# Kernel tuning notes

Measured on AMD Instinct MI355X. Metric: run time of the kernel, lower is better.

## Reference

```python
import jax, jax.numpy as jnp
import numpy as np

B, D, K = 8, 128, 7          # batch, num objects, per-object feature
Q = 256                      # question embedding size
G0, G1 = 511, 512            # g-layer sizes
F1, F2, OUT = 512, 1024, 16  # f-layer sizes


def setup_inputs() -> dict:
    key = jax.random.key(0)
    ks = jax.random.split(key, 14)
    def lin(kw, kb, fan_in, fan_out):
        lim = 1.0 / np.sqrt(fan_in)
        w = jax.random.uniform(kw, (fan_in, fan_out), jnp.float32, -lim, lim)
        b = jax.random.uniform(kb, (fan_out,), jnp.float32, -lim, lim)
        return w, b
    x = jax.random.normal(ks[0], (B, D, K), jnp.float32)
    qst = jax.random.normal(ks[1], (B, Q), jnp.float32)
    g0_w, g0_b = lin(ks[2], ks[3], 2 * K, G0)
    g1_w, g1_b = lin(ks[4], ks[5], G0 + Q, G1)
    f1_w, f1_b = lin(ks[6], ks[7], G1, F1)
    f2_w, f2_b = lin(ks[8], ks[9], F1, F2)
    f3_w, f3_b = lin(ks[10], ks[11], F2, OUT)
    return {"x": x, "qst": qst,
            "g0_w": g0_w, "g0_b": g0_b, "g1_w": g1_w, "g1_b": g1_b,
            "f1_w": f1_w, "f1_b": f1_b, "f2_w": f2_w, "f2_b": f2_b,
            "f3_w": f3_w, "f3_b": f3_b}


def reference(x, qst, g0_w, g0_b, g1_w, g1_b, f1_w, f1_b, f2_w, f2_b, f3_w, f3_b):
    b, d, k = x.shape
    # all-pairs: torch x_i[b,a,c,:]=x[b,c,:], x_j[b,a,c,:]=x[b,a,:]
    x_i = jnp.broadcast_to(x[:, None, :, :], (b, d, d, k))
    x_j = jnp.broadcast_to(x[:, :, None, :], (b, d, d, k))
    pairs = jnp.concatenate([x_i, x_j], axis=-1)            # (b,d,d,2k)
    h = jax.nn.relu(pairs @ g0_w + g0_b)                    # (b,d,d,G0)
    q = jnp.broadcast_to(qst[:, None, None, :], (b, d, d, qst.shape[-1]))
    h = jnp.concatenate([h, q], axis=-1)                    # (b,d,d,G0+Q)
    h = jax.nn.relu(h @ g1_w + g1_b)                        # (b,d,d,G1)
    x_g = h.sum(axis=(1, 2))                                # sum over d^2 pairs -> (b,G1)
    f = jax.nn.relu(x_g @ f1_w + f1_b)
    f = jax.nn.relu(f @ f2_w + f2_b)                        # dropout = identity (eval)
    logits = f @ f3_w + f3_b
    return jax.nn.log_softmax(logits, axis=1)
```

## Files before the change

kernel.cpp:

```cpp
#include <hip/hip_runtime.h>
#include <hip/hip_bf16.h>

#define B_  8
#define D_  128
#define K_  7
#define Q_  256
#define G0_ 511
#define G0P 512
#define G1_ 512
#define F1_ 512
#define F2_ 1024
#define OUT_ 16

typedef __bf16 bf16x8 __attribute__((ext_vector_type(8)));
typedef float  f32x4  __attribute__((ext_vector_type(4)));

#define GL2LDS(g, l) __builtin_amdgcn_global_load_lds(                        \
    (const __attribute__((address_space(1))) void*)(g),                       \
    (__attribute__((address_space(3))) void*)(l), 16, 0, 0)

__global__ void k_prep(const float* __restrict__ x, const float* __restrict__ g0w,
                       const float* __restrict__ g0b, const float* __restrict__ qst,
                       const float* __restrict__ g1w, const float* __restrict__ g1b,
                       const float* __restrict__ f1w, const float* __restrict__ f2w,
                       const float* __restrict__ f3w,
                       float* __restrict__ u, float* __restrict__ v,
                       __bf16* __restrict__ w1t, float* __restrict__ qterm,
                       float* __restrict__ xg, float* __restrict__ f1t,
                       float* __restrict__ f2t, float* __restrict__ f3t) {
    const int blk = blockIdx.x;
    const int t   = threadIdx.x;
    if (blk < 1024) {
        __shared__ float xs[8];
        if (t < K_) xs[t] = x[blk * K_ + t];
        __syncthreads();
        #pragma unroll
        for (int h = 0; h < 2; ++h) {
            const int g = t + h * 256;
            float su = 0.f, sv = 0.f;
            if (g < G0_) {
                #pragma unroll
                for (int k = 0; k < K_; ++k) {
                    su += xs[k] * g0w[k * G0_ + g];
                    sv += xs[k] * g0w[(K_ + k) * G0_ + g];
                }
                su += g0b[g];
            }
            u[blk * G0P + g] = (g < G0_) ? su : 0.f;
            v[blk * G0P + g] = (g < G0_) ? sv : 0.f;
        }
    } else if (blk < 1280) {
        __shared__ __bf16 tile[32][33];
        const int bb = blk - 1024;
        const int bx = bb & 15, by = bb >> 4;
        const int r = t >> 5, c = t & 31;
        #pragma unroll
        for (int i = 0; i < 4; ++i) {
            const int k = by * 32 + r + i * 8;
            const int n = bx * 32 + c;
            tile[r + i * 8][c] = (__bf16)((k < G0_) ? g1w[k * G1_ + n] : 0.f);
        }
        __syncthreads();
        #pragma unroll
        for (int i = 0; i < 4; ++i) {
            const int n = bx * 32 + r + i * 8;
            const int cc = (c >> 3) & 3, j = c & 7;
            const int slot = cc ^ ((n >> 1) & 3);
            w1t[by * 16384 + n * 32 + slot * 8 + j] = tile[c][r + i * 8];
        }
    } else if (blk < 1312) {
        __shared__ float qs[256];
        __shared__ float red[2][128];
        const int qb = blk - 1280;
        const int b = qb >> 2, nb = (qb & 3) << 7;
        qs[t] = qst[b * Q_ + t];
        __syncthreads();
        const int n = nb + (t & 127);
        const int qh = (t >> 7) * 128;
        float s = 0.f;
        #pragma unroll 8
        for (int q = 0; q < 128; ++q)
            s += qs[qh + q] * g1w[(G0_ + qh + q) * G1_ + n];
        red[t >> 7][t & 127] = s;
        __syncthreads();
        if (t < 128)
            qterm[b * G1_ + nb + t] = red[0][t] + red[1][t] + g1b[nb + t];
    } else if (blk < 1320) {
        const int b = blk - 1312;
        xg[b * G1_ + t] = 0.f;
        xg[b * G1_ + 256 + t] = 0.f;
    } else if (blk < 1576) {
        __shared__ float tile[32][33];
        const int j = blk - 1320;
        const int bo = j & 15, bk = j >> 4;
        const int r = t >> 5, c = t & 31;
        #pragma unroll
        for (int i = 0; i < 4; ++i)
            tile[r + i * 8][c] = f1w[(bk * 32 + r + i * 8) * F1_ + bo * 32 + c];
        __syncthreads();
        #pragma unroll
        for (int i = 0; i < 4; ++i)
            f1t[(bo * 32 + r + i * 8) * G1_ + bk * 32 + c] = tile[c][r + i * 8];
    } else if (blk < 2088) {
        __shared__ float tile[32][33];
        const int j = blk - 1576;
        const int bo = j & 31, bk = j >> 5;
        const int r = t >> 5, c = t & 31;
        #pragma unroll
        for (int i = 0; i < 4; ++i)
            tile[r + i * 8][c] = f2w[(bk * 32 + r + i * 8) * F2_ + bo * 32 + c];
        __syncthreads();
        #pragma unroll
        for (int i = 0; i < 4; ++i)
            f2t[(bo * 32 + r + i * 8) * F1_ + bk * 32 + c] = tile[c][r + i * 8];
    } else {
        const int k = (blk - 2088) * 256 + t;
        float4 r0 = *(const float4*)(f3w + k * OUT_);
        float4 r1 = *(const float4*)(f3w + k * OUT_ + 4);
        float4 r2 = *(const float4*)(f3w + k * OUT_ + 8);
        float4 r3 = *(const float4*)(f3w + k * OUT_ + 12);
        const float rr[16] = {r0.x,r0.y,r0.z,r0.w, r1.x,r1.y,r1.z,r1.w,
                              r2.x,r2.y,r2.z,r2.w, r3.x,r3.y,r3.z,r3.w};
        #pragma unroll
        for (int o = 0; o < 16; ++o) f3t[o * F2_ + k] = rr[o];
    }
}

__global__ __launch_bounds__(512, 4)
void k_pair(const float* __restrict__ u, const float* __restrict__ v,
            const __bf16* __restrict__ w1t, const float* __restrict__ qterm,
            float* __restrict__ xg) {
    __shared__ float  v_a[512];
    __shared__ __bf16 At[2][4096];
    __shared__ __bf16 Bt[3][8192];
    __shared__ float  ebuf[8][64];

    const int bid  = blockIdx.x;
    const int b    = bid >> 8;
    const int a    = (bid >> 1) & 127;
    const int nbase = (bid & 1) << 8;
    const int tid  = threadIdx.x;
    const int wave = tid >> 6, lane = tid & 63;
    const int quad = lane >> 4, l15 = lane & 15;
    const int wm   = wave >> 2;
    const int wn   = wave & 3;
    const int nloc = wn * 64;
    const int mtg  = wm * 4;
    const int swz  = (l15 >> 1) & 3;

    const int iw0 = wave * 2;
    const __bf16* gsrc = w1t + (size_t)(nbase + iw0 * 16 + (lane >> 2)) * 32
                             + (lane & 3) * 8;

    const int sm = tid >> 2;
    const int q8 = tid & 3;
    const float* urow = u + (size_t)(b * D_ + sm) * G0P + q8 * 8;
    const int woff = ((sm >> 4) * 512 + q8 * 128 + (sm & 15) * 8)
                   ^ (((q8 << 1) | ((sm >> 3) & 1)) << 3);
    const int afoff = (lane ^ (lane >> 3)) * 8;

    f32x4 acc[4][4];
    #pragma unroll
    for (int mt = 0; mt < 4; ++mt)
        #pragma unroll
        for (int nt = 0; nt < 4; ++nt)
            acc[mt][nt] = (f32x4){0.f, 0.f, 0.f, 0.f};

    float4 ua, ub;
    auto load_u = [&](int kq) {
        const float* p = urow + kq * 32;
        ua = *(const float4*)p;
        ub = *(const float4*)(p + 4);
    };
    auto stage_B = [&](int buf, int kq) {
        const __bf16* g = gsrc + (size_t)kq * 16384;
        __bf16* l = &Bt[buf][iw0 * 512];
        GL2LDS(g, l);
        GL2LDS(g + 512, l + 512);
    };
    auto write_A = [&](int buf, int kq) {
        const float* vp = v_a + kq * 32 + q8 * 8;
        const float4 va = *(const float4*)vp;
        const float4 vb = *(const float4*)(vp + 4);
        bf16x8 h;
        h[0] = (__bf16)fmaxf(ua.x + va.x, 0.f);
        h[1] = (__bf16)fmaxf(ua.y + va.y, 0.f);
        h[2] = (__bf16)fmaxf(ua.z + va.z, 0.f);
        h[3] = (__bf16)fmaxf(ua.w + va.w, 0.f);
        h[4] = (__bf16)fmaxf(ub.x + vb.x, 0.f);
        h[5] = (__bf16)fmaxf(ub.y + vb.y, 0.f);
        h[6] = (__bf16)fmaxf(ub.z + vb.z, 0.f);
        h[7] = (__bf16)fmaxf(ub.w + vb.w, 0.f);
        *(bf16x8*)&At[buf][woff] = h;
    };

    float4 vq;
    if (tid < 128) vq = *(const float4*)(v + (b * D_ + a) * G0P + tid * 4);
    load_u(0);
    asm volatile("" ::: "memory");
    stage_B(0, 0);
    stage_B(1, 1);
    if (tid < 128) *(float4*)(v_a + tid * 4) = vq;
    asm volatile("s_waitcnt lgkmcnt(0)\n\ts_barrier" ::: "memory");
    write_A(0, 0);
    asm volatile("s_waitcnt vmcnt(2) lgkmcnt(0)\n\ts_barrier" ::: "memory");

    int bcur = 0, bnxt = 1, bstg = 2;
    for (int kq = 0; kq < 16; ++kq) {
        const int abuf = kq & 1;
        if (kq < 15) load_u(kq + 1);
        asm volatile("" ::: "memory");
        if (kq < 14) stage_B(bstg, kq + 2);

        bf16x8 af[4];
        const __bf16* atb = &At[abuf][mtg * 512 + afoff];
        #pragma unroll
        for (int mt = 0; mt < 4; ++mt)
            af[mt] = *(const bf16x8*)(atb + mt * 512);
        bf16x8 bfr[4];
        const __bf16* btb = &Bt[bcur][(nloc + l15) * 32 + ((quad ^ swz) << 3)];
        #pragma unroll
        for (int nt = 0; nt < 4; ++nt)
            bfr[nt] = *(const bf16x8*)(btb + nt * 512);
        __builtin_amdgcn_s_setprio(1);
        #pragma unroll
        for (int mt = 0; mt < 4; ++mt)
            #pragma unroll
            for (int nt = 0; nt < 4; ++nt)
                acc[mt][nt] = __builtin_amdgcn_mfma_f32_16x16x32_bf16(
                    af[mt], bfr[nt], acc[mt][nt], 0, 0, 0);
        __builtin_amdgcn_s_setprio(0);

        if (kq < 15) write_A(abuf ^ 1, kq + 1);
        asm volatile("s_waitcnt lgkmcnt(0)\n\ts_barrier" ::: "memory");
        const int t3 = bcur; bcur = bnxt; bnxt = bstg; bstg = t3;
    }

    #pragma unroll
    for (int nt = 0; nt < 4; ++nt) {
        const float q = qterm[b * G1_ + nbase + nloc + nt * 16 + l15];
        float s = 0.f;
        #pragma unroll
        for (int mt = 0; mt < 4; ++mt)
            #pragma unroll
            for (int r = 0; r < 4; ++r)
                s += fmaxf(acc[mt][nt][r] + q, 0.f);
        s += __shfl_xor(s, 16, 64);
        s += __shfl_xor(s, 32, 64);
        if (quad == 0) ebuf[wave][nt * 16 + l15] = s;
    }
    __syncthreads();
    if (tid < 256) {
        const float sv = ebuf[tid >> 6][tid & 63] + ebuf[4 + (tid >> 6)][tid & 63];
        atomicAdd(xg + b * G1_ + nbase + tid, sv);
    }
}

__global__ void k_f1(const float* __restrict__ xg, const float* __restrict__ f1t,
                     const float* __restrict__ f1b, float* __restrict__ s1g) {
    const int wave = threadIdx.x >> 6, lane = threadIdx.x & 63;
    const int id = blockIdx.x * 4 + wave;
    const int b = id >> 9, oo = id & 511;
    const float* xr = xg + b * G1_ + lane * 8;
    const float* wr = f1t + oo * G1_ + lane * 8;
    const float4 a0 = *(const float4*)xr, a1 = *(const float4*)(xr + 4);
    const float4 b0 = *(const float4*)wr, b1 = *(const float4*)(wr + 4);
    float s = a0.x*b0.x + a0.y*b0.y + a0.z*b0.z + a0.w*b0.w
            + a1.x*b1.x + a1.y*b1.y + a1.z*b1.z + a1.w*b1.w;
    #pragma unroll
    for (int off = 32; off >= 1; off >>= 1) s += __shfl_xor(s, off, 64);
    if (lane == 0) s1g[b * F1_ + oo] = fmaxf(s + f1b[oo], 0.f);
}

__global__ void k_f2(const float* __restrict__ s1g, const float* __restrict__ f2t,
                     const float* __restrict__ f2b, float* __restrict__ s2g) {
    const int wave = threadIdx.x >> 6, lane = threadIdx.x & 63;
    const int id = blockIdx.x * 4 + wave;
    const int b = id >> 10, oo = id & 1023;
    const float* xr = s1g + b * F1_ + lane * 8;
    const float* wr = f2t + oo * F1_ + lane * 8;
    const float4 a0 = *(const float4*)xr, a1 = *(const float4*)(xr + 4);
    const float4 b0 = *(const float4*)wr, b1 = *(const float4*)(wr + 4);
    float s = a0.x*b0.x + a0.y*b0.y + a0.z*b0.z + a0.w*b0.w
            + a1.x*b1.x + a1.y*b1.y + a1.z*b1.z + a1.w*b1.w;
    #pragma unroll
    for (int off = 32; off >= 1; off >>= 1) s += __shfl_xor(s, off, 64);
    if (lane == 0) s2g[b * F2_ + oo] = fmaxf(s + f2b[oo], 0.f);
}

__global__ void k_f3(const float* __restrict__ s2g, const float* __restrict__ f3t,
                     const float* __restrict__ f3b, float* __restrict__ out) {
    const int b = blockIdx.x, t = threadIdx.x;
    const int wave = t >> 6, lane = t & 63;
    __shared__ float lg[16];
    float4 xs[4];
    #pragma unroll
    for (int j = 0; j < 4; ++j)
        xs[j] = *(const float4*)(s2g + b * F2_ + lane * 16 + j * 4);
    #pragma unroll
    for (int oi = 0; oi < 4; ++oi) {
        const int o = wave * 4 + oi;
        const float* wr = f3t + o * F2_ + lane * 16;
        float s = 0.f;
        #pragma unroll
        for (int j = 0; j < 4; ++j) {
            const float4 w = *(const float4*)(wr + j * 4);
            s += xs[j].x*w.x + xs[j].y*w.y + xs[j].z*w.z + xs[j].w*w.w;
        }
        #pragma unroll
        for (int off = 32; off >= 1; off >>= 1) s += __shfl_xor(s, off, 64);
        if (lane == 0) lg[o] = s + f3b[o];
    }
    __syncthreads();
    if (t < 16) {
        float m = -1e30f;
        #pragma unroll
        for (int i = 0; i < 16; ++i) m = fmaxf(m, lg[i]);
        float se = 0.f;
        #pragma unroll
        for (int i = 0; i < 16; ++i) se += __expf(lg[i] - m);
        out[b * OUT_ + t] = lg[t] - m - logf(se);
    }
}

extern "C" void kernel_launch(void* const* d_in, const int* in_sizes, int n_in,
                              void* d_out, int out_size, void* d_ws, size_t ws_size,
                              hipStream_t stream) {
    const float* x   = (const float*)d_in[0];
    const float* qst = (const float*)d_in[1];
    const float* g0w = (const float*)d_in[2];
    const float* g0b = (const float*)d_in[3];
    const float* g1w = (const float*)d_in[4];
    const float* g1b = (const float*)d_in[5];
    const float* f1w = (const float*)d_in[6];
    const float* f1b = (const float*)d_in[7];
    const float* f2w = (const float*)d_in[8];
    const float* f2b = (const float*)d_in[9];
    const float* f3w = (const float*)d_in[10];
    const float* f3b = (const float*)d_in[11];

    char* ws = (char*)d_ws;
    float*  u     = (float*)ws;  ws += (size_t)B_ * D_ * G0P * 4;
    float*  v     = (float*)ws;  ws += (size_t)B_ * D_ * G0P * 4;
    __bf16* w1t   = (__bf16*)ws; ws += (size_t)G1_ * G0P * 2;
    float*  qterm = (float*)ws;  ws += (size_t)B_ * G1_ * 4;
    float*  xg    = (float*)ws;  ws += (size_t)B_ * G1_ * 4;
    float*  s1g   = (float*)ws;  ws += (size_t)B_ * F1_ * 4;
    float*  s2g   = (float*)ws;  ws += (size_t)B_ * F2_ * 4;
    float*  f1t   = (float*)ws;  ws += (size_t)F1_ * G1_ * 4;
    float*  f2t   = (float*)ws;  ws += (size_t)F2_ * F1_ * 4;
    float*  f3t   = (float*)ws;  ws += (size_t)OUT_ * F2_ * 4;

    k_prep<<<2092, 256, 0, stream>>>(x, g0w, g0b, qst, g1w, g1b, f1w, f2w, f3w,
                                     u, v, w1t, qterm, xg, f1t, f2t, f3t);
    k_pair<<<B_ * D_ * 2, 512, 0, stream>>>(u, v, w1t, qterm, xg);
    k_f1  <<<1024, 256, 0, stream>>>(xg, f1t, f1b, s1g);
    k_f2  <<<2048, 256, 0, stream>>>(s1g, f2t, f2b, s2g);
    k_f3  <<<B_, 256, 0, stream>>>(s2g, f3t, f3b, (float*)d_out);
}
```

Measured before the change: 172.9 us.

## Fuse f1/f2/f3 tail kernels into one cooperative kernel with grid sync

Replaces the three small MLP-tail launches with a single cooperative kernel of 128 blocks of 1024 threads that runs f1, grid-syncs, runs f2, grid-syncs, then computes f3 and the log-softmax in 8 blocks. The aim is to remove the launch gaps and per-kernel drain between the tiny tail stages. In exchange it adds grid-wide barrier cost and fewer waves per stage, and it relies on cooperative launch support and all blocks being co-resident.

Measured after the change: 228.6 us. +32.2%, slower.

```diff
diff --git a/kernel.cpp b/kernel.cpp
--- a/kernel.cpp
+++ b/kernel.cpp
@@ -1,5 +1,7 @@
 #include <hip/hip_runtime.h>
 #include <hip/hip_bf16.h>
+#include <hip/hip_cooperative_groups.h>
+namespace cg = cooperative_groups;
 
 #define B_  8
 #define D_  128
@@ -256,70 +258,76 @@
     }
 }
 
-__global__ void k_f1(const float* __restrict__ xg, const float* __restrict__ f1t,
-                     const float* __restrict__ f1b, float* __restrict__ s1g) {
-    const int wave = threadIdx.x >> 6, lane = threadIdx.x & 63;
-    const int id = blockIdx.x * 4 + wave;
-    const int b = id >> 9, oo = id & 511;
-    const float* xr = xg + b * G1_ + lane * 8;
-    const float* wr = f1t + oo * G1_ + lane * 8;
-    const float4 a0 = *(const float4*)xr, a1 = *(const float4*)(xr + 4);
-    const float4 b0 = *(const float4*)wr, b1 = *(const float4*)(wr + 4);
-    float s = a0.x*b0.x + a0.y*b0.y + a0.z*b0.z + a0.w*b0.w
-            + a1.x*b1.x + a1.y*b1.y + a1.z*b1.z + a1.w*b1.w;
+__global__ __launch_bounds__(1024)
+void k_ftail(const float* __restrict__ xg,
+             const float* __restrict__ f1t, const float* __restrict__ f1b,
+             const float* __restrict__ f2t, const float* __restrict__ f2b,
+             const float* __restrict__ f3t, const float* __restrict__ f3b,
+             float* __restrict__ s1g, float* __restrict__ s2g,
+             float* __restrict__ out) {
+    cg::grid_group grid = cg::this_grid();
+    const int tid  = threadIdx.x;
+    const int wave = tid >> 6, lane = tid & 63;
+    const int gw   = blockIdx.x * 16 + wave;
+
     #pragma unroll
-    for (int off = 32; off >= 1; off >>= 1) s += __shfl_xor(s, off, 64);
-    if (lane == 0) s1g[b * F1_ + oo] = fmaxf(s + f1b[oo], 0.f);
-}
-
-__global__ void k_f2(const float* __restrict__ s1g, const float* __restrict__ f2t,
-                     const float* __restrict__ f2b, float* __restrict__ s2g) {
-    const int wave = threadIdx.x >> 6, lane = threadIdx.x & 63;
-    const int id = blockIdx.x * 4 + wave;
-    const int b = id >> 10, oo = id & 1023;
-    const float* xr = s1g + b * F1_ + lane * 8;
-    const float* wr = f2t + oo * F1_ + lane * 8;
-    const float4 a0 = *(const float4*)xr, a1 = *(const float4*)(xr + 4);
-    const float4 b0 = *(const float4*)wr, b1 = *(const float4*)(wr + 4);
-    float s = a0.x*b0.x + a0.y*b0.y + a0.z*b0.z + a0.w*b0.w
-            + a1.x*b1.x + a1.y*b1.y + a1.z*b1.z + a1.w*b1.w;
+    for (int r = 0; r < 2; ++r) {
+        const int id = gw + r * 2048;
+        const int b = id >> 9, oo = id & 511;
+        const float* xr = xg + b * G1_ + lane * 8;
+        const float* wr = f1t + (size_t)oo * G1_ + lane * 8;
+        const float4 a0 = *(const float4*)xr, a1 = *(const float4*)(xr + 4);
+        const float4 b0 = *(const float4*)wr, b1 = *(const float4*)(wr + 4);
+        float s = a0.x*b0.x + a0.y*b0.y + a0.z*b0.z + a0.w*b0.w
+                + a1.x*b1.x + a1.y*b1.y + a1.z*b1.z + a1.w*b1.w;
+        #pragma unroll
+        for (int off = 32; off >= 1; off >>= 1) s += __shfl_xor(s, off, 64);
+        if (lane == 0) s1g[b * F1_ + oo] = fmaxf(s + f1b[oo], 0.f);
+    }
+    grid.sync();
+
     #pragma unroll
-    for (int off = 32; off >= 1; off >>= 1) s += __shfl_xor(s, off, 64);
-    if (lane == 0) s2g[b * F2_ + oo] = fmaxf(s + f2b[oo], 0.f);
-}
-
-__global__ void k_f3(const float* __restrict__ s2g, const float* __restrict__ f3t,
-                     const float* __restrict__ f3b, float* __restrict__ out) {
-    const int b = blockIdx.x, t = threadIdx.x;
-    const int wave = t >> 6, lane = t & 63;
-    __shared__ float lg[16];
-    float4 xs[4];
-    #pragma unroll
-    for (int j = 0; j < 4; ++j)
-        xs[j] = *(const float4*)(s2g + b * F2_ + lane * 16 + j * 4);
-    #pragma unroll
-    for (int oi = 0; oi < 4; ++oi) {
-        const int o = wave * 4 + oi;
-        const float* wr = f3t + o * F2_ + lane * 16;
+    for (int r = 0; r < 4; ++r) {
+        const int id = gw + r * 2048;
+        const int b = id >> 10, oo = id & 1023;
+        const float* xr = s1g + b * F1_ + lane * 8;
+        const float* wr = f2t + (size_t)oo * F1_ + lane * 8;
+        const float4 a0 = *(const float4*)xr, a1 = *(const float4*)(xr + 4);
+        const float4 b0 = *(const float4*)wr, b1 = *(const float4*)(wr + 4);
+        float s = a0.x*b0.x + a0.y*b0.y + a0.z*b0.z + a0.w*b0.w
+                + a1.x*b1.x + a1.y*b1.y + a1.z*b1.z + a1.w*b1.w;
+        #pragma unroll
+        for (int off = 32; off >= 1; off >>= 1) s += __shfl_xor(s, off, 64);
+        if (lane == 0) s2g[b * F2_ + oo] = fmaxf(s + f2b[oo], 0.f);
+    }
+    grid.sync();
+
+    if (blockIdx.x < 8) {
+        const int b = blockIdx.x;
+        __shared__ float lg[16];
+        const int o = wave;
+        const float* xr = s2g + b * F2_ + lane * 16;
+        const float* wr = f3t + (size_t)o * F2_ + lane * 16;
         float s = 0.f;
         #pragma unroll
         for (int j = 0; j < 4; ++j) {
-            const float4 w = *(const float4*)(wr + j * 4);
-            s += xs[j].x*w.x + xs[j].y*w.y + xs[j].z*w.z + xs[j].w*w.w;
+            const float4 xv = *(const float4*)(xr + j * 4);
+            const float4 wv = *(const float4*)(wr + j * 4);
+            s += xv.x*wv.x + xv.y*wv.y + xv.z*wv.z + xv.w*wv.w;
         }
         #pragma unroll
         for (int off = 32; off >= 1; off >>= 1) s += __shfl_xor(s, off, 64);
         if (lane == 0) lg[o] = s + f3b[o];
-    }
-    __syncthreads();
-    if (t < 16) {
-        float m = -1e30f;
-        #pragma unroll
-        for (int i = 0; i < 16; ++i) m = fmaxf(m, lg[i]);
-        float se = 0.f;
-        #pragma unroll
-        for (int i = 0; i < 16; ++i) se += __expf(lg[i] - m);
-        out[b * OUT_ + t] = lg[t] - m - logf(se);
+        __syncthreads();
+        if (tid < 16) {
+            float m = -1e30f;
+            #pragma unroll
+            for (int i = 0; i < 16; ++i) m = fmaxf(m, lg[i]);
+            float se = 0.f;
+            #pragma unroll
+            for (int i = 0; i < 16; ++i) se += __expf(lg[i] - m);
+            out[b * OUT_ + tid] = lg[tid] - m - logf(se);
+        }
     }
 }
 
@@ -354,7 +362,11 @@
     k_prep<<<2092, 256, 0, stream>>>(x, g0w, g0b, qst, g1w, g1b, f1w, f2w, f3w,
                                      u, v, w1t, qterm, xg, f1t, f2t, f3t);
     k_pair<<<B_ * D_ * 2, 512, 0, stream>>>(u, v, w1t, qterm, xg);
-    k_f1  <<<1024, 256, 0, stream>>>(xg, f1t, f1b, s1g);
-    k_f2  <<<2048, 256, 0, stream>>>(s1g, f2t, f2b, s2g);
-    k_f3  <<<B_, 256, 0, stream>>>(s2g, f3t, f3b, (float*)d_out);
+
+    float* outp = (float*)d_out;
+    void* args[] = {(void*)&xg, (void*)&f1t, (void*)&f1b, (void*)&f2t,
+                    (void*)&f2b, (void*)&f3t, (void*)&f3b, (void*)&s1g,
+                    (void*)&s2g, (void*)&outp};
+    hipLaunchCooperativeKernel((const void*)k_ftail, dim3(128), dim3(1024),
+                               args, 0, stream);
 }
```
